# Optimization experiments

Hardware: AMD Instinct MI355X
Metric: run time of the kernel (lower is better)

Reference implementation:

```python
import jax, jax.numpy as jnp
import numpy as np

B, IN, HID, OUT = 1024, 512, 128, 64
INP1 = IN + 1  # 513, after prepending ones column


def setup_inputs() -> dict:
    key = jax.random.key(0)
    k1, k2, k3, k4, k5, k6, k7, k8 = jax.random.split(key, 8)
    s1 = 1.0 / np.sqrt(INP1 * INP1)
    s2 = 1.0 / np.sqrt(HID)
    return {
        "img": jax.random.normal(k1, (B, IN), dtype=jnp.float32),
        "tab": jax.random.normal(k2, (B, IN), dtype=jnp.float32),
        "W1": jax.random.uniform(k3, (HID, INP1 * INP1), jnp.float32, -s1, s1),
        "b1": jax.random.uniform(k4, (HID,), jnp.float32, -s1, s1),
        "W2": jax.random.uniform(k5, (HID, HID), jnp.float32, -s2, s2),
        "b2": jax.random.uniform(k6, (HID,), jnp.float32, -s2, s2),
        "W3": jax.random.uniform(k7, (OUT, HID), jnp.float32, -s2, s2),
        "b3": jax.random.uniform(k8, (OUT,), jnp.float32, -s2, s2),
    }


def reference(img, tab, W1, b1, W2, b2, W3, b3):
    ones = jnp.ones((img.shape[0], 1), dtype=img.dtype)
    x = jnp.concatenate([ones, img], axis=1)  # [B, IN+1]
    t = jnp.concatenate([ones, tab], axis=1)  # [B, IN+1]
    # batched outer product, flattened: [B, (IN+1)*(IN+1)]
    fusion = jnp.einsum("bi,bj->bij", x, t).reshape(x.shape[0], -1)
    # dropout is identity in eval mode
    y1 = fusion @ W1.T + b1
    y2 = jnp.tanh(y1 @ W2.T + b2)
    y3 = jax.nn.relu(y2 @ W3.T + b3)
    return y3
```

## Files before the change

### kernel.cpp

```cpp
#include <hip/hip_runtime.h>
#include <hip/hip_bf16.h>

typedef __bf16 bf16x8 __attribute__((ext_vector_type(8)));
typedef float f32x4 __attribute__((ext_vector_type(4)));
typedef float f32x4u __attribute__((ext_vector_type(4), aligned(4)));
typedef unsigned short u16x8 __attribute__((ext_vector_type(8)));

typedef __attribute__((address_space(1))) const unsigned int gu32;
typedef __attribute__((address_space(3))) unsigned int lu32;

#define B_SZ   1024
#define IN_SZ  512
#define HID    128
#define OUT_SZ 64
#define BK     32
#define NKT    16

static __device__ __forceinline__ unsigned short f2bf(float f) {
    __hip_bfloat16 h = __float2bfloat16(f);
    return *reinterpret_cast<unsigned short*>(&h);
}

__global__ __launch_bounds__(256) void prep_kernel(
    const float* __restrict__ img, const float* __restrict__ tab,
    unsigned short* __restrict__ tbt, float* __restrict__ xhT,
    float* __restrict__ tc)
{
    const int blk = blockIdx.x;
    for (int j = threadIdx.x; j < 512; j += 256) {
        float v = (j == 0) ? 1.0f : tab[(size_t)blk * IN_SZ + (j - 1)];
        tbt[(size_t)blk * 512 + j] = f2bf(v);
    }
    if (threadIdx.x == 0) tc[blk] = tab[(size_t)blk * IN_SZ + 511];
    if (blk < 513) {
        for (int b = threadIdx.x; b < B_SZ; b += 256)
            xhT[(size_t)blk * B_SZ + b] =
                (blk == 0) ? 1.0f : img[(size_t)b * IN_SZ + (blk - 1)];
    }
}

__global__ __launch_bounds__(256) void prep2_kernel(
    const float* __restrict__ w1, unsigned short* __restrict__ w1b)
{
    const long long gid = (long long)blockIdx.x * 256 + threadIdx.x;
    const int r  = (int)(gid >> 6);
    const int c8 = ((int)gid & 63) << 3;
    const float* src = w1 + (size_t)r * 513 + c8;
    const f32x4u lo = *reinterpret_cast<const f32x4u*>(src);
    const f32x4u hi = *reinterpret_cast<const f32x4u*>(src + 4);
    u16x8 u;
    u[0] = f2bf(lo[0]); u[1] = f2bf(lo[1]); u[2] = f2bf(lo[2]); u[3] = f2bf(lo[3]);
    u[4] = f2bf(hi[0]); u[5] = f2bf(hi[1]); u[6] = f2bf(hi[2]); u[7] = f2bf(hi[3]);
    *reinterpret_cast<u16x8*>(w1b + (size_t)r * 512 + c8) = u;
}

__global__ __launch_bounds__(512, 4) void gemm_fused(
    const float* __restrict__ w1, const unsigned short* __restrict__ w1b,
    const unsigned short* __restrict__ tbt,
    const float* __restrict__ xhT, const float* __restrict__ tc,
    float* __restrict__ y1acc)
{
    __shared__ unsigned short Als[2][128 * BK];
    __shared__ unsigned short Bls[2][256 * BK];

    const int bm = blockIdx.x >> 2;
    const int bn = blockIdx.x & 3;
    const int m0 = bm * 128;
    const int n0 = bn * 256;
    const int tid  = threadIdx.x;
    const int wv   = tid >> 6;
    const int wr   = wv >> 2;
    const int wc   = wv & 3;
    const int lane = tid & 63;
    const int l15  = lane & 15;
    const int kg   = lane >> 4;

    const unsigned short* asrc;
    {
        const int r  = tid >> 2;
        const int cl = (tid & 3) ^ ((r >> 1) & 3);
        asrc = w1b + (size_t)(m0 + r) * 512 + cl * 8;
    }
    const int aBase = (wv * 64) * 8;

    const unsigned short* bsrc[2];
    int bBase[2];
    #pragma unroll
    for (int q = 0; q < 2; ++q) {
        const int p  = q * 512 + tid;
        const int r  = p >> 2;
        const int cl = (p & 3) ^ ((r >> 1) & 3);
        bsrc[q] = tbt + (size_t)(n0 + r) * 512 + cl * 8;
        bBase[q] = (q * 512 + wv * 64) * 8;
    }

    int aoffs[4], boffs[4];
    #pragma unroll
    for (int ms = 0; ms < 4; ++ms) {
        const int r = wr * 64 + ms * 16 + l15;
        aoffs[ms] = (r * 4 + (kg ^ ((r >> 1) & 3))) * 8;
    }
    #pragma unroll
    for (int ns = 0; ns < 4; ++ns) {
        const int r = wc * 64 + ns * 16 + l15;
        boffs[ns] = (r * 4 + (kg ^ ((r >> 1) & 3))) * 8;
    }

    f32x4 acc[4][4] = {};

#define STAGE(BUF, KT) do {                                                  \
        const int k32_ = (KT) * BK;                                          \
        __builtin_amdgcn_global_load_lds(                                    \
            (gu32*)(const void*)(asrc + k32_),                               \
            (lu32*)(void*)&Als[BUF][aBase], 16, 0, 0);                       \
        _Pragma("unroll")                                                    \
        for (int q_ = 0; q_ < 2; ++q_)                                       \
            __builtin_amdgcn_global_load_lds(                                \
                (gu32*)(const void*)(bsrc[q_] + k32_),                       \
                (lu32*)(void*)&Bls[BUF][bBase[q_]], 16, 0, 0);               \
    } while (0)

    STAGE(0, 0);
    __syncthreads();

    for (int kt = 0; kt < NKT; ++kt) {
        const int cur = kt & 1;
        if (kt + 1 < NKT) STAGE(cur ^ 1, kt + 1);

        const unsigned short* ab = &Als[cur][0];
        const unsigned short* bb = &Bls[cur][0];
        bf16x8 af[4], bfr[4];
        #pragma unroll
        for (int ms = 0; ms < 4; ++ms)
            af[ms] = *reinterpret_cast<const bf16x8*>(&ab[aoffs[ms]]);
        #pragma unroll
        for (int ns = 0; ns < 4; ++ns)
            bfr[ns] = *reinterpret_cast<const bf16x8*>(&bb[boffs[ns]]);
        #pragma unroll
        for (int ms = 0; ms < 4; ++ms)
            #pragma unroll
            for (int ns = 0; ns < 4; ++ns)
                acc[ms][ns] = __builtin_amdgcn_mfma_f32_16x16x32_bf16(
                    af[ms], bfr[ns], acc[ms][ns], 0, 0, 0);
        __syncthreads();
    }
#undef STAGE

    const int h0 = m0 / 513;
    const int mb = (h0 + 1) * 513;
    const bool cross = (mb < m0 + 128);

    float wcv[4][4];
    #pragma unroll
    for (int ms = 0; ms < 4; ++ms)
        #pragma unroll
        for (int v = 0; v < 4; ++v)
            wcv[ms][v] = w1[(size_t)(m0 + wr * 64 + ms * 16 + kg * 4 + v) * 513 + 512];

    #pragma unroll
    for (int ns = 0; ns < 4; ++ns) {
        const int ncol = n0 + wc * 64 + ns * 16 + l15;
        const float tv = tc[ncol];
        float s0 = 0.f, s1 = 0.f;
        #pragma unroll
        for (int ms = 0; ms < 4; ++ms) {
            #pragma unroll
            for (int v = 0; v < 4; ++v) {
                const int m = m0 + wr * 64 + ms * 16 + kg * 4 + v;
                const bool lo = (m < mb);
                const int i = lo ? (m - h0 * 513) : (m - mb);
                const float xv = xhT[(size_t)i * B_SZ + ncol];
                const float val = (acc[ms][ns][v] + wcv[ms][v] * tv) * xv;
                if (lo) s0 += val; else s1 += val;
            }
        }
        s0 += __shfl_xor(s0, 16); s0 += __shfl_xor(s0, 32);
        if (lane < 16) atomicAdd(&y1acc[(size_t)ncol * HID + h0], s0);
        if (cross) {
            s1 += __shfl_xor(s1, 16); s1 += __shfl_xor(s1, 32);
            if (lane < 16 && (h0 + 1) < HID)
                atomicAdd(&y1acc[(size_t)ncol * HID + h0 + 1], s1);
        }
    }
}

__global__ __launch_bounds__(512, 4) void gemm_fused_fb(
    const float* __restrict__ w1, const unsigned short* __restrict__ tbt,
    const float* __restrict__ xhT, const float* __restrict__ tc,
    float* __restrict__ y1acc)
{
    __shared__ float          Afs[2][64 * BK];
    __shared__ unsigned short Bls[2][512 * BK];

    const int bm = blockIdx.x >> 1;
    const int bn = blockIdx.x & 1;
    const int m0 = bm * 64;
    const int n0 = bn * 512;
    const int tid  = threadIdx.x;
    const int wv   = tid >> 6;
    const int lane = tid & 63;
    const int l15  = lane & 15;
    const int kg   = lane >> 4;

    const int ar  = tid >> 3;
    const int acl = (tid & 7) ^ (ar & 7);
    const float* asrc = w1 + (size_t)(m0 + ar) * 513 + acl * 4;
    const int aBase = (wv * 64) * 4;

    const unsigned short* bsrc[4];
    int bBase[4];
    #pragma unroll
    for (int q = 0; q < 4; ++q) {
        const int p  = q * 512 + tid;
        const int r  = p >> 2;
        const int cl = (p & 3) ^ ((r >> 1) & 3);
        bsrc[q] = tbt + (size_t)(n0 + r) * 512 + cl * 8;
        bBase[q] = (q * 512 + wv * 64) * 8;
    }

    int aoff0[4], aoff1[4], boffs[4];
    #pragma unroll
    for (int ms = 0; ms < 4; ++ms) {
        const int r = ms * 16 + l15;
        aoff0[ms] = r * 32 + (((kg * 2) + 0) ^ (r & 7)) * 4;
        aoff1[ms] = r * 32 + (((kg * 2) + 1) ^ (r & 7)) * 4;
    }
    #pragma unroll
    for (int ns = 0; ns < 4; ++ns) {
        const int r = wv * 64 + ns * 16 + l15;
        boffs[ns] = ((r << 2) | (kg ^ ((r >> 1) & 3))) * 8;
    }

    f32x4 acc[4][4] = {};

#define STAGE_FB(BUF, KT) do {                                               \
        const int k32_ = (KT) * BK;                                          \
        _Pragma("unroll")                                                    \
        for (int q_ = 0; q_ < 4; ++q_)                                       \
            __builtin_amdgcn_global_load_lds(                                \
                (gu32*)(const void*)(bsrc[q_] + k32_),                       \
                (lu32*)(void*)&Bls[BUF][bBase[q_]], 16, 0, 0);               \
        __builtin_amdgcn_global_load_lds(                                    \
            (gu32*)(const void*)(asrc + k32_),                               \
            (lu32*)(void*)&Afs[BUF][aBase], 16, 0, 0);                       \
    } while (0)

    STAGE_FB(0, 0);
    __syncthreads();

    for (int kt = 0; kt < NKT; ++kt) {
        const int cur = kt & 1;
        if (kt + 1 < NKT) STAGE_FB(cur ^ 1, kt + 1);

        const float*          ab = &Afs[cur][0];
        const unsigned short* bb = &Bls[cur][0];
        bf16x8 bfr[4];
        #pragma unroll
        for (int ns = 0; ns < 4; ++ns)
            bfr[ns] = *reinterpret_cast<const bf16x8*>(&bb[boffs[ns]]);
        #pragma unroll
        for (int ms = 0; ms < 4; ++ms) {
            const f32x4 lo = *reinterpret_cast<const f32x4*>(&ab[aoff0[ms]]);
            const f32x4 hi = *reinterpret_cast<const f32x4*>(&ab[aoff1[ms]]);
            u16x8 u;
            u[0] = f2bf(lo[0]); u[1] = f2bf(lo[1]);
            u[2] = f2bf(lo[2]); u[3] = f2bf(lo[3]);
            u[4] = f2bf(hi[0]); u[5] = f2bf(hi[1]);
            u[6] = f2bf(hi[2]); u[7] = f2bf(hi[3]);
            const bf16x8 af = __builtin_bit_cast(bf16x8, u);
            #pragma unroll
            for (int ns = 0; ns < 4; ++ns)
                acc[ms][ns] = __builtin_amdgcn_mfma_f32_16x16x32_bf16(
                    af, bfr[ns], acc[ms][ns], 0, 0, 0);
        }
        __syncthreads();
    }
#undef STAGE_FB

    const int h0 = m0 / 513;
    const int mb = (h0 + 1) * 513;
    const bool cross = (mb < m0 + 64);

    float wcv[4][4];
    #pragma unroll
    for (int ms = 0; ms < 4; ++ms)
        #pragma unroll
        for (int v = 0; v < 4; ++v)
            wcv[ms][v] = w1[(size_t)(m0 + ms * 16 + kg * 4 + v) * 513 + 512];

    #pragma unroll
    for (int ns = 0; ns < 4; ++ns) {
        const int ncol = n0 + wv * 64 + ns * 16 + l15;
        const float tv = tc[ncol];
        float s0 = 0.f, s1 = 0.f;
        #pragma unroll
        for (int ms = 0; ms < 4; ++ms) {
            #pragma unroll
            for (int v = 0; v < 4; ++v) {
                const int m = m0 + ms * 16 + kg * 4 + v;
                const bool lo = (m < mb);
                const int i = lo ? (m - h0 * 513) : (m - mb);
                const float xv = xhT[(size_t)i * B_SZ + ncol];
                const float val = (acc[ms][ns][v] + wcv[ms][v] * tv) * xv;
                if (lo) s0 += val; else s1 += val;
            }
        }
        s0 += __shfl_xor(s0, 16); s0 += __shfl_xor(s0, 32);
        if (lane < 16) atomicAdd(&y1acc[(size_t)ncol * HID + h0], s0);
        if (cross) {
            s1 += __shfl_xor(s1, 16); s1 += __shfl_xor(s1, 32);
            if (lane < 16 && (h0 + 1) < HID)
                atomicAdd(&y1acc[(size_t)ncol * HID + h0 + 1], s1);
        }
    }
}

__global__ __launch_bounds__(128) void mlp_kernel(
    const float* __restrict__ y1acc, const float* __restrict__ b1,
    const float* __restrict__ W2, const float* __restrict__ b2,
    const float* __restrict__ W3, const float* __restrict__ b3,
    float* __restrict__ out)
{
    __shared__ float y1r[HID];
    __shared__ float y2r[HID];
    const int b = blockIdx.x;
    const int h = threadIdx.x;
    y1r[h] = y1acc[(size_t)b * HID + h] + b1[h];
    __syncthreads();
    float a = b2[h];
    const float* w2r = W2 + (size_t)h * HID;
    #pragma unroll 8
    for (int k = 0; k < HID; ++k) a += w2r[k] * y1r[k];
    y2r[h] = tanhf(a);
    __syncthreads();
    if (h < OUT_SZ) {
        float a3 = b3[h];
        const float* w3r = W3 + (size_t)h * HID;
        #pragma unroll 8
        for (int k = 0; k < HID; ++k) a3 += w3r[k] * y2r[k];
        out[(size_t)b * OUT_SZ + h] = fmaxf(a3, 0.f);
    }
}

extern "C" void kernel_launch(void* const* d_in, const int* in_sizes, int n_in,
                              void* d_out, int out_size, void* d_ws, size_t ws_size,
                              hipStream_t stream) {
    const float* img = (const float*)d_in[0];
    const float* tab = (const float*)d_in[1];
    const float* W1  = (const float*)d_in[2];
    const float* b1  = (const float*)d_in[3];
    const float* W2  = (const float*)d_in[4];
    const float* b2  = (const float*)d_in[5];
    const float* W3  = (const float*)d_in[6];
    const float* b3  = (const float*)d_in[7];
    float* out = (float*)d_out;

    char* ws = (char*)d_ws;
    float*          y1acc = (float*)ws;
    unsigned short* tbt   = (unsigned short*)(ws + 524288);
    float*          xhT   = (float*)(ws + 1572864);
    float*          tc    = (float*)(ws + 3674112);
    unsigned short* w1b   = (unsigned short*)(ws + 3678208);
    const size_t need = 3678208ULL + 67239936ULL;

    hipMemsetAsync(y1acc, 0, (size_t)B_SZ * HID * sizeof(float), stream);
    prep_kernel<<<dim3(1024), dim3(256), 0, stream>>>(img, tab, tbt, xhT, tc);
    if (ws_size >= need) {
        prep2_kernel<<<dim3(65664 * 64 / 256), dim3(256), 0, stream>>>(W1, w1b);
        gemm_fused<<<dim3(2052), dim3(512), 0, stream>>>(W1, w1b, tbt, xhT, tc, y1acc);
    } else {
        gemm_fused_fb<<<dim3(2052), dim3(512), 0, stream>>>(W1, tbt, xhT, tc, y1acc);
    }
    mlp_kernel<<<dim3(1024), dim3(128), 0, stream>>>(y1acc, b1, W2, b2, W3, b3, out);
}
```

Before: 205.9 us.

## Make main GEMM persistent with atomic tile scheduler and triple-buffered prefetch

```diff
diff --git a/kernel.cpp b/kernel.cpp
--- a/kernel.cpp
+++ b/kernel.cpp
@@ -3,6 +3,7 @@
 
 typedef __bf16 bf16x8 __attribute__((ext_vector_type(8)));
 typedef float f32x4 __attribute__((ext_vector_type(4)));
+typedef float f32x4a __attribute__((ext_vector_type(4), aligned(4)));
 typedef float f32x4u __attribute__((ext_vector_type(4), aligned(4)));
 typedef unsigned short u16x8 __attribute__((ext_vector_type(8)));
 
@@ -15,6 +16,10 @@
 #define OUT_SZ 64
 #define BK     32
 #define NKT    16
+#define NTILES 2052
+#define GRID   512
+#define ABUF   4096
+#define BBUF   8192
 
 static __device__ __forceinline__ unsigned short f2bf(float f) {
     __hip_bfloat16 h = __float2bfloat16(f);
@@ -23,7 +28,7 @@
 
 __global__ __launch_bounds__(256) void prep_kernel(
     const float* __restrict__ img, const float* __restrict__ tab,
-    unsigned short* __restrict__ tbt, float* __restrict__ xhT,
+    unsigned short* __restrict__ tbt, float* __restrict__ xh,
     float* __restrict__ tc)
 {
     const int blk = blockIdx.x;
@@ -32,11 +37,9 @@
         tbt[(size_t)blk * 512 + j] = f2bf(v);
     }
     if (threadIdx.x == 0) tc[blk] = tab[(size_t)blk * IN_SZ + 511];
-    if (blk < 513) {
-        for (int b = threadIdx.x; b < B_SZ; b += 256)
-            xhT[(size_t)blk * B_SZ + b] =
-                (blk == 0) ? 1.0f : img[(size_t)b * IN_SZ + (blk - 1)];
-    }
+    for (int j = threadIdx.x; j < 513; j += 256)
+        xh[(size_t)blk * 513 + j] =
+            (j == 0) ? 1.0f : img[(size_t)blk * IN_SZ + (j - 1)];
 }
 
 __global__ __launch_bounds__(256) void prep2_kernel(
@@ -57,16 +60,13 @@
 __global__ __launch_bounds__(512, 4) void gemm_fused(
     const float* __restrict__ w1, const unsigned short* __restrict__ w1b,
     const unsigned short* __restrict__ tbt,
-    const float* __restrict__ xhT, const float* __restrict__ tc,
-    float* __restrict__ y1acc)
+    const float* __restrict__ xh, const float* __restrict__ tc,
+    float* __restrict__ y1acc, int* __restrict__ ctr)
 {
-    __shared__ unsigned short Als[2][128 * BK];
-    __shared__ unsigned short Bls[2][256 * BK];
-
-    const int bm = blockIdx.x >> 2;
-    const int bn = blockIdx.x & 3;
-    const int m0 = bm * 128;
-    const int n0 = bn * 256;
+    __shared__ unsigned short Als[3 * ABUF];
+    __shared__ unsigned short Bls[3 * BBUF];
+    __shared__ int sNxt;
+
     const int tid  = threadIdx.x;
     const int wv   = tid >> 6;
     const int wr   = wv >> 2;
@@ -75,22 +75,18 @@
     const int l15  = lane & 15;
     const int kg   = lane >> 4;
 
-    const unsigned short* asrc;
-    {
-        const int r  = tid >> 2;
-        const int cl = (tid & 3) ^ ((r >> 1) & 3);
-        asrc = w1b + (size_t)(m0 + r) * 512 + cl * 8;
-    }
+    const int ar  = tid >> 2;
+    const int acl = (tid & 3) ^ ((ar >> 1) & 3);
+    const size_t aRC = (size_t)ar * 512 + acl * 8;
     const int aBase = (wv * 64) * 8;
 
-    const unsigned short* bsrc[2];
-    int bBase[2];
+    size_t bRC[2]; int bBase[2];
     #pragma unroll
     for (int q = 0; q < 2; ++q) {
         const int p  = q * 512 + tid;
         const int r  = p >> 2;
         const int cl = (p & 3) ^ ((r >> 1) & 3);
-        bsrc[q] = tbt + (size_t)(n0 + r) * 512 + cl * 8;
+        bRC[q]   = (size_t)r * 512 + cl * 8;
         bBase[q] = (q * 512 + wv * 64) * 8;
     }
 
@@ -106,87 +102,147 @@
         boffs[ns] = (r * 4 + (kg ^ ((r >> 1) & 3))) * 8;
     }
 
-    f32x4 acc[4][4] = {};
-
-#define STAGE(BUF, KT) do {                                                  \
-        const int k32_ = (KT) * BK;                                          \
+#define STAGE(OS, SA, SB, KK) do {                                           \
         __builtin_amdgcn_global_load_lds(                                    \
-            (gu32*)(const void*)(asrc + k32_),                               \
-            (lu32*)(void*)&Als[BUF][aBase], 16, 0, 0);                       \
+            (gu32*)(const void*)((SA) + (KK) * 32),                          \
+            (lu32*)(void*)&Als[(OS) * ABUF + aBase], 16, 0, 0);              \
         _Pragma("unroll")                                                    \
         for (int q_ = 0; q_ < 2; ++q_)                                       \
             __builtin_amdgcn_global_load_lds(                                \
-                (gu32*)(const void*)(bsrc[q_] + k32_),                       \
-                (lu32*)(void*)&Bls[BUF][bBase[q_]], 16, 0, 0);               \
+                (gu32*)(const void*)(tbt + (SB) + bRC[q_] + (KK) * 32),      \
+                (lu32*)(void*)&Bls[(OS) * BBUF + bBase[q_]], 16, 0, 0);      \
     } while (0)
 
-    STAGE(0, 0);
-    __syncthreads();
-
-    for (int kt = 0; kt < NKT; ++kt) {
-        const int cur = kt & 1;
-        if (kt + 1 < NKT) STAGE(cur ^ 1, kt + 1);
-
-        const unsigned short* ab = &Als[cur][0];
-        const unsigned short* bb = &Bls[cur][0];
-        bf16x8 af[4], bfr[4];
+    int curT = blockIdx.x;
+    const unsigned short* sA = w1b + (size_t)(curT >> 2) * 65536 + aRC;
+    size_t sB = (size_t)(curT & 3) * 131072;
+    int oc = 0, on = 1, os = 2;
+    STAGE(0, sA, sB, 0);
+    STAGE(1, sA, sB, 1);
+
+    f32x4 acc[4][4] = {};
+    bool avail = false;
+    int ntReg = NTILES;
+
+    for (;;) {
+        const int m0 = (curT >> 2) * 128;
+        const int n0 = (curT & 3) * 256;
+
         #pragma unroll
-        for (int ms = 0; ms < 4; ++ms)
-            af[ms] = *reinterpret_cast<const bf16x8*>(&ab[aoffs[ms]]);
-        #pragma unroll
-        for (int ns = 0; ns < 4; ++ns)
-            bfr[ns] = *reinterpret_cast<const bf16x8*>(&bb[boffs[ns]]);
-        #pragma unroll
-        for (int ms = 0; ms < 4; ++ms)
+        for (int kt = 0; kt < NKT; ++kt) {
+            if (kt == NKT - 1 && !avail)
+                asm volatile("s_waitcnt vmcnt(0)" ::: "memory");
+            else
+                asm volatile("s_waitcnt vmcnt(3)" ::: "memory");
+            __builtin_amdgcn_s_barrier();
+            __builtin_amdgcn_sched_barrier(0);
+
+            if (kt < 14) {
+                STAGE(os, sA, sB, kt + 2);
+            } else if (kt == 14) {
+                ntReg = sNxt;
+                avail = (ntReg < NTILES);
+                if (avail) {
+                    sA = w1b + (size_t)(ntReg >> 2) * 65536 + aRC;
+                    sB = (size_t)(ntReg & 3) * 131072;
+                    STAGE(os, sA, sB, 0);
+                }
+            } else {
+                if (avail) STAGE(os, sA, sB, 1);
+            }
+
+            if (kt == 10 && tid == 0)
+                sNxt = GRID + atomicAdd(ctr, 1);
+
+            const unsigned short* ab = &Als[oc * ABUF];
+            const unsigned short* bb = &Bls[oc * BBUF];
+            bf16x8 af[4], bfr[4];
+            #pragma unroll
+            for (int ms = 0; ms < 4; ++ms)
+                af[ms] = *reinterpret_cast<const bf16x8*>(&ab[aoffs[ms]]);
             #pragma unroll
             for (int ns = 0; ns < 4; ++ns)
-                acc[ms][ns] = __builtin_amdgcn_mfma_f32_16x16x32_bf16(
-                    af[ms], bfr[ns], acc[ms][ns], 0, 0, 0);
-        __syncthreads();
+                bfr[ns] = *reinterpret_cast<const bf16x8*>(&bb[boffs[ns]]);
+            __builtin_amdgcn_s_setprio(1);
+            #pragma unroll
+            for (int ms = 0; ms < 4; ++ms)
+                #pragma unroll
+                for (int ns = 0; ns < 4; ++ns)
+                    acc[ms][ns] = __builtin_amdgcn_mfma_f32_16x16x32_bf16(
+                        af[ms], bfr[ns], acc[ms][ns], 0, 0, 0);
+            __builtin_amdgcn_s_setprio(0);
+
+            const int t_ = oc; oc = on; on = os; os = t_;
+        }
+
+        {
+            const int h0 = m0 / 513;
+            const int mb = (h0 + 1) * 513;
+            const bool cross = (mb < m0 + 128);
+
+            float wcv[4][4];
+            #pragma unroll
+            for (int ms = 0; ms < 4; ++ms)
+                #pragma unroll
+                for (int v = 0; v < 4; ++v)
+                    wcv[ms][v] =
+                        w1[(size_t)(m0 + wr * 64 + ms * 16 + kg * 4 + v) * 513 + 512];
+
+            #pragma unroll
+            for (int ns = 0; ns < 4; ++ns) {
+                const int ncol = n0 + wc * 64 + ns * 16 + l15;
+                const float tv = tc[ncol];
+                const float* xrow = xh + (size_t)ncol * 513;
+                float s0 = 0.f, s1 = 0.f;
+                #pragma unroll
+                for (int ms = 0; ms < 4; ++ms) {
+                    const int mbase = m0 + wr * 64 + ms * 16 + kg * 4;
+                    f32x4 c = acc[ms][ns];
+                    c[0] += wcv[ms][0] * tv; c[1] += wcv[ms][1] * tv;
+                    c[2] += wcv[ms][2] * tv; c[3] += wcv[ms][3] * tv;
+                    if (mbase + 3 < mb) {
+                        const f32x4a xv =
+                            *reinterpret_cast<const f32x4a*>(xrow + (mbase - h0 * 513));
+                        s0 += c[0]*xv[0] + c[1]*xv[1] + c[2]*xv[2] + c[3]*xv[3];
+                    } else if (mbase >= mb) {
+                        const f32x4a xv =
+                            *reinterpret_cast<const f32x4a*>(xrow + (mbase - mb));
+                        s1 += c[0]*xv[0] + c[1]*xv[1] + c[2]*xv[2] + c[3]*xv[3];
+                    } else {
+                        #pragma unroll
+                        for (int v = 0; v < 4; ++v) {
+                            const int m = mbase + v;
+                            const bool lo = (m < mb);
+                            const int i = lo ? (m - h0 * 513) : (m - mb);
+                            const float val = c[v] * xrow[i];
+                            if (lo) s0 += val; else s1 += val;
+                        }
+                    }
+                }
+                s0 += __shfl_xor(s0, 16); s0 += __shfl_xor(s0, 32);
+                if (lane < 16) atomicAdd(&y1acc[(size_t)ncol * HID + h0], s0);
+                if (cross) {
+                    s1 += __shfl_xor(s1, 16); s1 += __shfl_xor(s1, 32);
+                    if (lane < 16 && (h0 + 1) < HID)
+                        atomicAdd(&y1acc[(size_t)ncol * HID + h0 + 1], s1);
+                }
+            }
+            #pragma unroll
+            for (int ms = 0; ms < 4; ++ms)
+                #pragma unroll
+                for (int ns = 0; ns < 4; ++ns)
+                    acc[ms][ns] = (f32x4){0.f, 0.f, 0.f, 0.f};
+        }
+
+        if (!avail) break;
+        curT = ntReg;
     }
 #undef STAGE
-
-    const int h0 = m0 / 513;
-    const int mb = (h0 + 1) * 513;
-    const bool cross = (mb < m0 + 128);
-
-    float wcv[4][4];
-    #pragma unroll
-    for (int ms = 0; ms < 4; ++ms)
-        #pragma unroll
-        for (int v = 0; v < 4; ++v)
-            wcv[ms][v] = w1[(size_t)(m0 + wr * 64 + ms * 16 + kg * 4 + v) * 513 + 512];
-
-    #pragma unroll
-    for (int ns = 0; ns < 4; ++ns) {
-        const int ncol = n0 + wc * 64 + ns * 16 + l15;
-        const float tv = tc[ncol];
-        float s0 = 0.f, s1 = 0.f;
-        #pragma unroll
-        for (int ms = 0; ms < 4; ++ms) {
-            #pragma unroll
-            for (int v = 0; v < 4; ++v) {
-                const int m = m0 + wr * 64 + ms * 16 + kg * 4 + v;
-                const bool lo = (m < mb);
-                const int i = lo ? (m - h0 * 513) : (m - mb);
-                const float xv = xhT[(size_t)i * B_SZ + ncol];
-                const float val = (acc[ms][ns][v] + wcv[ms][v] * tv) * xv;
-                if (lo) s0 += val; else s1 += val;
-            }
-        }
-        s0 += __shfl_xor(s0, 16); s0 += __shfl_xor(s0, 32);
-        if (lane < 16) atomicAdd(&y1acc[(size_t)ncol * HID + h0], s0);
-        if (cross) {
-            s1 += __shfl_xor(s1, 16); s1 += __shfl_xor(s1, 32);
-            if (lane < 16 && (h0 + 1) < HID)
-                atomicAdd(&y1acc[(size_t)ncol * HID + h0 + 1], s1);
-        }
-    }
 }
 
 __global__ __launch_bounds__(512, 4) void gemm_fused_fb(
     const float* __restrict__ w1, const unsigned short* __restrict__ tbt,
-    const float* __restrict__ xhT, const float* __restrict__ tc,
+    const float* __restrict__ xh, const float* __restrict__ tc,
     float* __restrict__ y1acc)
 {
     __shared__ float          Afs[2][64 * BK];
@@ -292,6 +348,7 @@
     for (int ns = 0; ns < 4; ++ns) {
         const int ncol = n0 + wv * 64 + ns * 16 + l15;
         const float tv = tc[ncol];
+        const float* xrow = xh + (size_t)ncol * 513;
         float s0 = 0.f, s1 = 0.f;
         #pragma unroll
         for (int ms = 0; ms < 4; ++ms) {
@@ -300,8 +357,7 @@
                 const int m = m0 + ms * 16 + kg * 4 + v;
                 const bool lo = (m < mb);
                 const int i = lo ? (m - h0 * 513) : (m - mb);
-                const float xv = xhT[(size_t)i * B_SZ + ncol];
-                const float val = (acc[ms][ns][v] + wcv[ms][v] * tv) * xv;
+                const float val = (acc[ms][ns][v] + wcv[ms][v] * tv) * xrow[i];
                 if (lo) s0 += val; else s1 += val;
             }
         }
@@ -358,18 +414,20 @@
     char* ws = (char*)d_ws;
     float*          y1acc = (float*)ws;
     unsigned short* tbt   = (unsigned short*)(ws + 524288);
-    float*          xhT   = (float*)(ws + 1572864);
+    float*          xh    = (float*)(ws + 1572864);
     float*          tc    = (float*)(ws + 3674112);
-    unsigned short* w1b   = (unsigned short*)(ws + 3678208);
-    const size_t need = 3678208ULL + 67239936ULL;
+    int*            ctr   = (int*)(ws + 3678208);
+    unsigned short* w1b   = (unsigned short*)(ws + 3678224);
+    const size_t need = 3678224ULL + 67239936ULL;
 
     hipMemsetAsync(y1acc, 0, (size_t)B_SZ * HID * sizeof(float), stream);
-    prep_kernel<<<dim3(1024), dim3(256), 0, stream>>>(img, tab, tbt, xhT, tc);
+    hipMemsetAsync(ctr, 0, 16, stream);
+    prep_kernel<<<dim3(1024), dim3(256), 0, stream>>>(img, tab, tbt, xh, tc);
     if (ws_size >= need) {
         prep2_kernel<<<dim3(65664 * 64 / 256), dim3(256), 0, stream>>>(W1, w1b);
-        gemm_fused<<<dim3(2052), dim3(512), 0, stream>>>(W1, w1b, tbt, xhT, tc, y1acc);
+        gemm_fused<<<dim3(GRID), dim3(512), 0, stream>>>(W1, w1b, tbt, xh, tc, y1acc, ctr);
     } else {
-        gemm_fused_fb<<<dim3(2052), dim3(512), 0, stream>>>(W1, tbt, xhT, tc, y1acc);
+        gemm_fused_fb<<<dim3(2052), dim3(512), 0, stream>>>(W1, tbt, xh, tc, y1acc);
     }
     mlp_kernel<<<dim3(1024), dim3(128), 0, stream>>>(y1acc, b1, W2, b2, W3, b3, out);
 }
```

Measured after the change: 239.4 us. 1.16x slower.
